# Kernel optimization log

Hardware: AMD Instinct MI355X
Metric: run time of the kernel (lower is better)

The kernel has to match this reference:

```python
import jax, jax.numpy as jnp
import numpy as np

GMIN = 0.01
GMAX = 10.0


def _ptanh(x, eta):
    # printed tanh-style learnable activation: eta0 + eta1 * tanh((x - eta2) * eta3)
    return eta[0] + eta[1] * jnp.tanh((x - eta[2]) * eta[3])


def setup_inputs() -> dict:
    key = jax.random.key(0)
    k1, k2 = jax.random.split(key)
    B, n_in, n_out = 32768, 256, 256
    a_previous = jax.random.uniform(k1, (B, n_in), dtype=jnp.float32)
    eta_act = jnp.array([0.0, 1.0, 0.5, 2.0], dtype=jnp.float32)
    eta_inv = jnp.array([1.0, -1.0, 0.5, 2.0], dtype=jnp.float32)
    # theta init exactly as in pLayer.__init__
    theta = jax.random.uniform(k2, (n_in + 2, n_out), dtype=jnp.float32) / 100.0 + GMIN
    theta = theta.at[-1, :].add(GMAX)
    ratio = eta_act[2] / (1.0 - eta_act[2])  # eta2/(1-eta2)
    theta = theta.at[-2, :].set(ratio * (jnp.sum(theta[:-2, :], axis=0) + theta[-1, :]))
    return {"a_previous": a_previous, "theta_": theta, "eta_act": eta_act, "eta_inv": eta_inv}


def reference(a_previous, theta_, eta_act, eta_inv):
    # clamp + threshold-to-zero (forward value of the straight-through theta)
    theta = jnp.clip(theta_, -GMAX, GMAX)
    theta = jnp.where(jnp.abs(theta) < GMIN, 0.0, theta)
    # normalized conductance weights
    abs_t = jnp.abs(theta)
    W = abs_t / jnp.sum(abs_t, axis=0, keepdims=True)  # [n_in+2, n_out]
    pos = (theta >= 0.0).astype(theta.dtype)
    neg = 1.0 - pos
    B = a_previous.shape[0]
    ones = jnp.ones((B, 1), dtype=a_previous.dtype)
    zeros = jnp.zeros((B, 1), dtype=a_previous.dtype)
    a_ext = jnp.concatenate([a_previous, ones, zeros], axis=1)  # [B, n_in+2]
    a_neg = _ptanh(a_ext, eta_inv).at[:, -1].set(0.0)  # inverter, last (dummy) col zeroed
    z = a_ext @ (W * pos) + a_neg @ (W * neg)  # [B, n_out]
    return _ptanh(z, eta_act)
```

## Files before the change

### kernel.cpp

```cpp
#include <hip/hip_runtime.h>
#include <hip/hip_bf16.h>

typedef unsigned int u32;
typedef __attribute__((ext_vector_type(8))) _Float16 f16x8;
typedef __attribute__((ext_vector_type(4))) float f32x4;

#define GMIN_ 0.01f
#define GMAX_ 10.0f

__global__ __launch_bounds__(256) void prep_weights(
    const float* __restrict__ theta, const float* __restrict__ eta_inv,
    _Float16* __restrict__ W2t, float* __restrict__ bias)
{
    __shared__ float psum[16][16];
    const int t    = threadIdx.x;
    const int nloc = t & 15;
    const int kth  = t >> 4;
    const int n    = blockIdx.x * 16 + nloc;

    float partial = 0.f;
    for (int k = kth; k < 258; k += 16) {
        float tt = theta[k * 256 + n];
        tt = fminf(fmaxf(tt, -GMAX_), GMAX_);
        if (fabsf(tt) < GMIN_) tt = 0.f;
        partial += fabsf(tt);
    }
    psum[kth][nloc] = partial;
    __syncthreads();
    float s = 0.f;
#pragma unroll
    for (int j = 0; j < 16; ++j) s += psum[j][nloc];
    const float inv = 1.0f / s;

    for (int k = kth; k < 256; k += 16) {
        float tt = theta[k * 256 + n];
        tt = fminf(fmaxf(tt, -GMAX_), GMAX_);
        if (fabsf(tt) < GMIN_) tt = 0.f;
        float w  = fabsf(tt) * inv;
        float wp = (tt >= 0.f) ? w : 0.f;
        float wn = w - wp;
        union { _Float16 h[2]; u32 u; } p;
        p.h[0] = (_Float16)wp;
        p.h[1] = (_Float16)wn;
        *(u32*)((char*)W2t + (size_t)n * 1024 + (size_t)k * 4) = p.u;
    }

    if (kth == 0) {
        float tt = theta[256 * 256 + n];
        tt = fminf(fmaxf(tt, -GMAX_), GMAX_);
        if (fabsf(tt) < GMIN_) tt = 0.f;
        float w  = fabsf(tt) * inv;
        float wp = (tt >= 0.f) ? w : 0.f;
        float wn = w - wp;
        float ei0 = eta_inv[0], ei1 = eta_inv[1], ei2 = eta_inv[2], ei3 = eta_inv[3];
        float a1 = ei0 + ei1 * tanhf((1.0f - ei2) * ei3);
        bias[n] = wp + a1 * wn;
    }
}

__global__ __launch_bounds__(256) void plax_gemm(
    const float* __restrict__ A, const _Float16* __restrict__ W2t,
    const float* __restrict__ bias, const float* __restrict__ eta_act,
    const float* __restrict__ eta_inv, float* __restrict__ out)
{
    __shared__ __align__(16) char lds[32768];
    char* ldsB = lds + 16384;

    const int t    = threadIdx.x;
    const int bid  = blockIdx.x;
    const int sw   = ((bid & 7) << 6) | (bid >> 3);
    const int bm   = sw >> 1;
    const int bn   = sw & 1;
    const int lane = t & 63;
    const int wave = t >> 6;
    const int wr   = wave >> 1, wc = wave & 1;

    const float ei0 = eta_inv[0], ei1 = eta_inv[1], ei2 = eta_inv[2], ei3 = eta_inv[3];

    f32x4 acc[4][4] = {};

    const int r0 = t >> 3;
    const int c4 = t & 7;

    for (int kt = 0; kt < 8; ++kt) {
        __syncthreads();

#pragma unroll
        for (int i = 0; i < 4; ++i) {
            const int o  = i * 4096 + t * 16;
            const int r  = o >> 7;
            const int sl = (o >> 4) & 7;
            const int s0 = sl ^ (r & 7);
            const char* gp = (const char*)W2t
                + (size_t)(bn * 128 + r) * 1024 + (size_t)kt * 128 + (size_t)s0 * 16;
            __builtin_amdgcn_global_load_lds(
                (const __attribute__((address_space(1))) u32*)gp,
                (__attribute__((address_space(3))) u32*)(ldsB + o), 16, 0, 0);
        }

#pragma unroll
        for (int i = 0; i < 4; ++i) {
            const int r = r0 + 32 * i;
            const float4 v = *(const float4*)&A[(size_t)(bm * 128 + r) * 256 + kt * 32 + c4 * 4];
            f16x8 hv;
            const float xs0 = v.x, xs1 = v.y, xs2 = v.z, xs3 = v.w;
            hv[0] = (_Float16)xs0; hv[1] = (_Float16)(ei0 + ei1 * tanhf((xs0 - ei2) * ei3));
            hv[2] = (_Float16)xs1; hv[3] = (_Float16)(ei0 + ei1 * tanhf((xs1 - ei2) * ei3));
            hv[4] = (_Float16)xs2; hv[5] = (_Float16)(ei0 + ei1 * tanhf((xs2 - ei2) * ei3));
            hv[6] = (_Float16)xs3; hv[7] = (_Float16)(ei0 + ei1 * tanhf((xs3 - ei2) * ei3));
            const int s0 = c4 ^ (r & 7);
            *(f16x8*)(lds + (size_t)r * 128 + s0 * 16) = hv;
        }

        __syncthreads();

#pragma unroll
        for (int ks = 0; ks < 2; ++ks) {
            f16x8 af[4], bf[4];
#pragma unroll
            for (int m = 0; m < 4; ++m) {
                const int rr   = wr * 64 + m * 16 + (lane & 15);
                const int slot = (ks * 4 + (lane >> 4)) ^ (rr & 7);
                af[m] = *(const f16x8*)(lds + (size_t)rr * 128 + slot * 16);
            }
#pragma unroll
            for (int nn = 0; nn < 4; ++nn) {
                const int rr   = wc * 64 + nn * 16 + (lane & 15);
                const int slot = (ks * 4 + (lane >> 4)) ^ (rr & 7);
                bf[nn] = *(const f16x8*)(ldsB + (size_t)rr * 128 + slot * 16);
            }
#pragma unroll
            for (int m = 0; m < 4; ++m)
#pragma unroll
                for (int nn = 0; nn < 4; ++nn)
                    acc[m][nn] = __builtin_amdgcn_mfma_f32_16x16x32_f16(
                        af[m], bf[nn], acc[m][nn], 0, 0, 0);
        }
    }

    const float ea0 = eta_act[0], ea1 = eta_act[1], ea2 = eta_act[2], ea3 = eta_act[3];
    const int colbase = bn * 128 + wc * 64 + (lane & 15);
    float bcol[4];
#pragma unroll
    for (int nn = 0; nn < 4; ++nn) bcol[nn] = bias[colbase + nn * 16];

#pragma unroll
    for (int m = 0; m < 4; ++m) {
        const int rgb = bm * 128 + wr * 64 + m * 16 + (lane >> 4) * 4;
#pragma unroll
        for (int nn = 0; nn < 4; ++nn) {
            const int cg = colbase + nn * 16;
#pragma unroll
            for (int j = 0; j < 4; ++j) {
                const float z = acc[m][nn][j] + bcol[nn];
                out[(size_t)(rgb + j) * 256 + cg] = ea0 + ea1 * tanhf((z - ea2) * ea3);
            }
        }
    }
}

extern "C" void kernel_launch(void* const* d_in, const int* in_sizes, int n_in,
                              void* d_out, int out_size, void* d_ws, size_t ws_size,
                              hipStream_t stream) {
    (void)in_sizes; (void)n_in; (void)out_size; (void)ws_size;
    const float* a       = (const float*)d_in[0];
    const float* theta   = (const float*)d_in[1];
    const float* eta_act = (const float*)d_in[2];
    const float* eta_inv = (const float*)d_in[3];
    float* out = (float*)d_out;

    _Float16* W2t = (_Float16*)d_ws;
    float*    bias = (float*)((char*)d_ws + 256 * 512 * 2);

    prep_weights<<<16, 256, 0, stream>>>(theta, eta_inv, W2t, bias);
    plax_gemm<<<512, 256, 0, stream>>>(a, W2t, bias, eta_act, eta_inv, out);
}
```

Measured before the change: 132.2 us.

## Drop LDS staging, load MFMA fragments directly from global with register prefetch

The GEMM no longer stages A and W tiles in shared memory. Each wave loads its MFMA fragments straight from global memory into registers, prefetches the next k-step, and uses a 128x64 block tile over 1024 blocks with an occupancy hint. tanhf is replaced by an exp plus reciprocal approximation in both the inverter and the output activation. The weight-prep kernel is also reworked to one block per output column with a wave-shuffle reduction. Dropping LDS removes the barriers, but the same A and W data is now reloaded per wave from L2/global, and the fast tanh can overflow for large arguments.

```diff
diff --git a/kernel.cpp b/kernel.cpp
--- a/kernel.cpp
+++ b/kernel.cpp
@@ -8,152 +8,150 @@
 #define GMIN_ 0.01f
 #define GMAX_ 10.0f
 
+__device__ __forceinline__ float tanh_fast2(float y2) {
+    float e = __expf(y2);
+    float r = __builtin_amdgcn_rcpf(e + 1.0f);
+    return fmaf(-2.0f, r, 1.0f);
+}
+
 __global__ __launch_bounds__(256) void prep_weights(
     const float* __restrict__ theta, const float* __restrict__ eta_inv,
     _Float16* __restrict__ W2t, float* __restrict__ bias)
 {
-    __shared__ float psum[16][16];
-    const int t    = threadIdx.x;
-    const int nloc = t & 15;
-    const int kth  = t >> 4;
-    const int n    = blockIdx.x * 16 + nloc;
+    const int n = blockIdx.x;
+    const int t = threadIdx.x;
+    const int lane = t & 63, wave = t >> 6;
+    __shared__ float red[4];
 
-    float partial = 0.f;
-    for (int k = kth; k < 258; k += 16) {
-        float tt = theta[k * 256 + n];
-        tt = fminf(fmaxf(tt, -GMAX_), GMAX_);
-        if (fabsf(tt) < GMIN_) tt = 0.f;
-        partial += fabsf(tt);
-    }
-    psum[kth][nloc] = partial;
-    __syncthreads();
-    float s = 0.f;
-#pragma unroll
-    for (int j = 0; j < 16; ++j) s += psum[j][nloc];
-    const float inv = 1.0f / s;
+    float tt = theta[t * 256 + n];
+    tt = fminf(fmaxf(tt, -GMAX_), GMAX_);
+    if (fabsf(tt) < GMIN_) tt = 0.f;
 
-    for (int k = kth; k < 256; k += 16) {
-        float tt = theta[k * 256 + n];
-        tt = fminf(fmaxf(tt, -GMAX_), GMAX_);
-        if (fabsf(tt) < GMIN_) tt = 0.f;
-        float w  = fabsf(tt) * inv;
-        float wp = (tt >= 0.f) ? w : 0.f;
-        float wn = w - wp;
-        union { _Float16 h[2]; u32 u; } p;
-        p.h[0] = (_Float16)wp;
-        p.h[1] = (_Float16)wn;
-        *(u32*)((char*)W2t + (size_t)n * 1024 + (size_t)k * 4) = p.u;
+    float extra = 0.f;
+    if (t < 2) {
+        extra = theta[(256 + t) * 256 + n];
+        extra = fminf(fmaxf(extra, -GMAX_), GMAX_);
+        if (fabsf(extra) < GMIN_) extra = 0.f;
     }
 
-    if (kth == 0) {
-        float tt = theta[256 * 256 + n];
-        tt = fminf(fmaxf(tt, -GMAX_), GMAX_);
-        if (fabsf(tt) < GMIN_) tt = 0.f;
-        float w  = fabsf(tt) * inv;
-        float wp = (tt >= 0.f) ? w : 0.f;
-        float wn = w - wp;
-        float ei0 = eta_inv[0], ei1 = eta_inv[1], ei2 = eta_inv[2], ei3 = eta_inv[3];
-        float a1 = ei0 + ei1 * tanhf((1.0f - ei2) * ei3);
-        bias[n] = wp + a1 * wn;
+    float s = fabsf(tt) + fabsf(extra);
+#pragma unroll
+    for (int i = 32; i > 0; i >>= 1) s += __shfl_xor(s, i);
+    if (lane == 0) red[wave] = s;
+    __syncthreads();
+    const float inv = 1.0f / (red[0] + red[1] + red[2] + red[3]);
+
+    const float w  = fabsf(tt) * inv;
+    const float wp = (tt >= 0.f) ? w : 0.f;
+    const float wn = w - wp;
+    union { _Float16 h[2]; u32 u; } p;
+    p.h[0] = (_Float16)wp;
+    p.h[1] = (_Float16)wn;
+    *(u32*)((char*)W2t + (size_t)n * 1024 + (size_t)t * 4) = p.u;
+
+    if (t == 0) {
+        const float w6  = fabsf(extra) * inv;
+        const float wp6 = (extra >= 0.f) ? w6 : 0.f;
+        const float wn6 = w6 - wp6;
+        const float ei0 = eta_inv[0], ei1 = eta_inv[1], ei2 = eta_inv[2], ei3 = eta_inv[3];
+        const float a1  = ei0 + ei1 * tanhf((1.0f - ei2) * ei3);
+        bias[n] = wp6 + a1 * wn6;
     }
 }
 
-__global__ __launch_bounds__(256) void plax_gemm(
+__global__ __launch_bounds__(256, 4) void plax_gemm(
     const float* __restrict__ A, const _Float16* __restrict__ W2t,
     const float* __restrict__ bias, const float* __restrict__ eta_act,
     const float* __restrict__ eta_inv, float* __restrict__ out)
 {
-    __shared__ __align__(16) char lds[32768];
-    char* ldsB = lds + 16384;
-
     const int t    = threadIdx.x;
     const int bid  = blockIdx.x;
-    const int sw   = ((bid & 7) << 6) | (bid >> 3);
-    const int bm   = sw >> 1;
-    const int bn   = sw & 1;
-    const int lane = t & 63;
-    const int wave = t >> 6;
-    const int wr   = wave >> 1, wc = wave & 1;
+    const int swz  = ((bid & 7) << 7) | (bid >> 3);
+    const int mblk = swz >> 2;
+    const int nblk = swz & 3;
+    const int lane = t & 63, wave = t >> 6;
+    const int lr   = lane & 15, lg = lane >> 4;
 
-    const float ei0 = eta_inv[0], ei1 = eta_inv[1], ei2 = eta_inv[2], ei3 = eta_inv[3];
+    const float ei0 = eta_inv[0], ei1 = eta_inv[1];
+    const float k2i = 2.0f * eta_inv[3];
+    const float c2i = 2.0f * eta_inv[2] * eta_inv[3];
 
-    f32x4 acc[4][4] = {};
+    const int row0 = mblk * 128 + wave * 32;
+    const int col0 = nblk * 64;
 
-    const int r0 = t >> 3;
-    const int c4 = t & 7;
+    const float*    ap = A   + (size_t)(row0 + lr) * 256 + lg * 4;
+    const _Float16* bp = W2t + (size_t)(col0 + lr) * 512 + lg * 8;
 
-    for (int kt = 0; kt < 8; ++kt) {
-        __syncthreads();
+    f32x4 acc[2][4] = {};
+
+#define LD(ks, aa, bb) do {                                   \
+        aa[0] = *(const float4*)(ap + (ks) * 16);             \
+        aa[1] = *(const float4*)(ap + 4096 + (ks) * 16);      \
+        bb[0] = *(const f16x8*)(bp + (ks) * 32);              \
+        bb[1] = *(const f16x8*)(bp + 8192  + (ks) * 32);      \
+        bb[2] = *(const f16x8*)(bp + 16384 + (ks) * 32);      \
+        bb[3] = *(const f16x8*)(bp + 24576 + (ks) * 32);      \
+    } while (0)
+
+    float4 a4c[2]; f16x8 bfc[4];
+    LD(0, a4c, bfc);
 
 #pragma unroll
-        for (int i = 0; i < 4; ++i) {
-            const int o  = i * 4096 + t * 16;
-            const int r  = o >> 7;
-            const int sl = (o >> 4) & 7;
-            const int s0 = sl ^ (r & 7);
-            const char* gp = (const char*)W2t
-                + (size_t)(bn * 128 + r) * 1024 + (size_t)kt * 128 + (size_t)s0 * 16;
-            __builtin_amdgcn_global_load_lds(
-                (const __attribute__((address_space(1))) u32*)gp,
-                (__attribute__((address_space(3))) u32*)(ldsB + o), 16, 0, 0);
+    for (int ks = 0; ks < 16; ++ks) {
+        float4 a4n[2]; f16x8 bfn[4];
+        if (ks < 15) LD(ks + 1, a4n, bfn);
+
+        f16x8 af[2];
+#pragma unroll
+        for (int m = 0; m < 2; ++m) {
+            const float4 v = a4c[m];
+            f16x8 h;
+            h[0] = (_Float16)v.x;
+            h[1] = (_Float16)fmaf(ei1, tanh_fast2(fmaf(v.x, k2i, -c2i)), ei0);
+            h[2] = (_Float16)v.y;
+            h[3] = (_Float16)fmaf(ei1, tanh_fast2(fmaf(v.y, k2i, -c2i)), ei0);
+            h[4] = (_Float16)v.z;
+            h[5] = (_Float16)fmaf(ei1, tanh_fast2(fmaf(v.z, k2i, -c2i)), ei0);
+            h[6] = (_Float16)v.w;
+            h[7] = (_Float16)fmaf(ei1, tanh_fast2(fmaf(v.w, k2i, -c2i)), ei0);
+            af[m] = h;
         }
 
 #pragma unroll
-        for (int i = 0; i < 4; ++i) {
-            const int r = r0 + 32 * i;
-            const float4 v = *(const float4*)&A[(size_t)(bm * 128 + r) * 256 + kt * 32 + c4 * 4];
-            f16x8 hv;
-            const float xs0 = v.x, xs1 = v.y, xs2 = v.z, xs3 = v.w;
-            hv[0] = (_Float16)xs0; hv[1] = (_Float16)(ei0 + ei1 * tanhf((xs0 - ei2) * ei3));
-            hv[2] = (_Float16)xs1; hv[3] = (_Float16)(ei0 + ei1 * tanhf((xs1 - ei2) * ei3));
-            hv[4] = (_Float16)xs2; hv[5] = (_Float16)(ei0 + ei1 * tanhf((xs2 - ei2) * ei3));
-            hv[6] = (_Float16)xs3; hv[7] = (_Float16)(ei0 + ei1 * tanhf((xs3 - ei2) * ei3));
-            const int s0 = c4 ^ (r & 7);
-            *(f16x8*)(lds + (size_t)r * 128 + s0 * 16) = hv;
+        for (int m = 0; m < 2; ++m)
+#pragma unroll
+            for (int n = 0; n < 4; ++n)
+                acc[m][n] = __builtin_amdgcn_mfma_f32_16x16x32_f16(
+                    af[m], bfc[n], acc[m][n], 0, 0, 0);
+
+        if (ks < 15) {
+#pragma unroll
+            for (int m = 0; m < 2; ++m) a4c[m] = a4n[m];
+#pragma unroll
+            for (int n = 0; n < 4; ++n) bfc[n] = bfn[n];
         }
+    }
+#undef LD
 
-        __syncthreads();
+    const float ea0 = eta_act[0], ea1 = eta_act[1];
+    const float k2a = 2.0f * eta_act[3];
+    const float c2a = 2.0f * eta_act[2] * eta_act[3];
+
+    float bc[4];
+#pragma unroll
+    for (int n = 0; n < 4; ++n) bc[n] = bias[col0 + n * 16 + lr];
 
 #pragma unroll
-        for (int ks = 0; ks < 2; ++ks) {
-            f16x8 af[4], bf[4];
+    for (int m = 0; m < 2; ++m) {
+        const int rgb = row0 + m * 16 + lg * 4;
 #pragma unroll
-            for (int m = 0; m < 4; ++m) {
-                const int rr   = wr * 64 + m * 16 + (lane & 15);
-                const int slot = (ks * 4 + (lane >> 4)) ^ (rr & 7);
-                af[m] = *(const f16x8*)(lds + (size_t)rr * 128 + slot * 16);
-            }
-#pragma unroll
-            for (int nn = 0; nn < 4; ++nn) {
-                const int rr   = wc * 64 + nn * 16 + (lane & 15);
-                const int slot = (ks * 4 + (lane >> 4)) ^ (rr & 7);
-                bf[nn] = *(const f16x8*)(ldsB + (size_t)rr * 128 + slot * 16);
-            }
-#pragma unroll
-            for (int m = 0; m < 4; ++m)
-#pragma unroll
-                for (int nn = 0; nn < 4; ++nn)
-                    acc[m][nn] = __builtin_amdgcn_mfma_f32_16x16x32_f16(
-                        af[m], bf[nn], acc[m][nn], 0, 0, 0);
-        }
-    }
-
-    const float ea0 = eta_act[0], ea1 = eta_act[1], ea2 = eta_act[2], ea3 = eta_act[3];
-    const int colbase = bn * 128 + wc * 64 + (lane & 15);
-    float bcol[4];
-#pragma unroll
-    for (int nn = 0; nn < 4; ++nn) bcol[nn] = bias[colbase + nn * 16];
-
-#pragma unroll
-    for (int m = 0; m < 4; ++m) {
-        const int rgb = bm * 128 + wr * 64 + m * 16 + (lane >> 4) * 4;
-#pragma unroll
-        for (int nn = 0; nn < 4; ++nn) {
-            const int cg = colbase + nn * 16;
+        for (int n = 0; n < 4; ++n) {
+            const int cg = col0 + n * 16 + lr;
 #pragma unroll
             for (int j = 0; j < 4; ++j) {
-                const float z = acc[m][nn][j] + bcol[nn];
-                out[(size_t)(rgb + j) * 256 + cg] = ea0 + ea1 * tanhf((z - ea2) * ea3);
+                const float z = acc[m][n][j] + bc[n];
+                out[(size_t)(rgb + j) * 256 + cg] =
+                    fmaf(ea1, tanh_fast2(fmaf(z, k2a, -c2a)), ea0);
             }
         }
     }
@@ -169,9 +167,9 @@
     const float* eta_inv = (const float*)d_in[3];
     float* out = (float*)d_out;
 
-    _Float16* W2t = (_Float16*)d_ws;
+    _Float16* W2t  = (_Float16*)d_ws;
     float*    bias = (float*)((char*)d_ws + 256 * 512 * 2);
 
-    prep_weights<<<16, 256, 0, stream>>>(theta, eta_inv, W2t, bias);
-    plax_gemm<<<512, 256, 0, stream>>>(a, W2t, bias, eta_act, eta_inv, out);
+    prep_weights<<<256, 256, 0, stream>>>(theta, eta_inv, W2t, bias);
+    plax_gemm<<<1024, 256, 0, stream>>>(a, W2t, bias, eta_act, eta_inv, out);
 }
```

After: 129.2 us. -2.3%, faster.
